# Kernel tuning notes

Hardware: AMD Instinct MI355X
Metric: run time of the kernel (lower is better)

## Reference

```python
import jax, jax.numpy as jnp
import numpy as np

B, C, I, E = 2048, 256, 9, 10


def _contraction(U_list, W_list, x, y):
    """Recursive symmetric contraction for one output irrep.
    U_list/W_list ordered [U1, U2, U3] (correlation 1..3).
    x: [b, c, i], y: [b, e]. Returns flattened [b, c * m].
    """
    U3, W3 = U_list[-1], W_list[-1]
    # main: '...ik,ekc,bci,be->bc...'
    out = jnp.einsum('...ik,ekc,bci,be->bc...', U3, W3, x, y)
    for corr in range(len(U_list) - 2, -1, -1):
        U, W = U_list[corr], W_list[corr]
        # weighting: '...k,ekc,be->bc...'
        c_tensor = jnp.einsum('...k,ekc,be->bc...', U, W, y) + out
        # contract: 'bc...i,bci->bc...'
        out = jnp.einsum('bc...i,bci->bc...', c_tensor, x)
    return out.reshape(out.shape[0], -1)


def setup_inputs() -> dict:
    key = jax.random.key(0)
    ks = jax.random.split(key, 14)
    inp = {
        'x': jax.random.normal(ks[0], (B, C, I), jnp.float32),
        'y': jax.random.uniform(ks[1], (B, E), jnp.float32),
        'U1_s': jax.random.normal(ks[2], (I, 1), jnp.float32),
        'U2_s': jax.random.normal(ks[3], (I, I, 3), jnp.float32),
        'U3_s': jax.random.normal(ks[4], (I, I, I, 23), jnp.float32),
        'U1_v': jax.random.normal(ks[5], (3, I, 1), jnp.float32),
        'U2_v': jax.random.normal(ks[6], (3, I, I, 4), jnp.float32),
        'U3_v': jax.random.normal(ks[7], (3, I, I, I, 30), jnp.float32),
        'W1_s': jax.random.normal(ks[8], (E, 1, C), jnp.float32),
        'W2_s': jax.random.normal(ks[9], (E, 3, C), jnp.float32) / 3.0,
        'W3_s': jax.random.normal(ks[10], (E, 23, C), jnp.float32) / 23.0,
        'W1_v': jax.random.normal(ks[11], (E, 1, C), jnp.float32),
        'W2_v': jax.random.normal(ks[12], (E, 4, C), jnp.float32) / 4.0,
        'W3_v': jax.random.normal(ks[13], (E, 30, C), jnp.float32) / 30.0,
    }
    return inp


def reference(x, y, U1_s, U2_s, U3_s, U1_v, U2_v, U3_v,
              W1_s, W2_s, W3_s, W1_v, W2_v, W3_v):
    out_s = _contraction([U1_s, U2_s, U3_s], [W1_s, W2_s, W3_s], x, y)  # [b, c]
    out_v = _contraction([U1_v, U2_v, U3_v], [W1_v, W2_v, W3_v], x, y)  # [b, c*3]
    return jnp.concatenate([out_s, out_v], axis=-1)  # [b, 4c]
```

## Files before the change

### kernel.cpp

```cpp
#include <hip/hip_runtime.h>
#include <hip/hip_bf16.h>


#define NB 2048
#define NC 256
#define NI 9
#define NE 10

#define N_TRI 165
#define N_PAIR 45
#define BT 8

#define T3N (N_TRI * NE * NC)
#define T2N (N_PAIR * NE * NC)
#define T1N (NI * NE * NC)

__global__ __launch_bounds__(256) void sc_prep(
    const float* __restrict__ U1_s, const float* __restrict__ U2_s,
    const float* __restrict__ U3_s, const float* __restrict__ U1_v,
    const float* __restrict__ U2_v, const float* __restrict__ U3_v,
    const float* __restrict__ W1_s, const float* __restrict__ W2_s,
    const float* __restrict__ W3_s, const float* __restrict__ W1_v,
    const float* __restrict__ W2_v, const float* __restrict__ W3_v,
    float* __restrict__ ws)
{
    const int m = blockIdx.x;
    const int tid = threadIdx.x;
    float4* __restrict__ T3 = (float4*)ws;
    float4* __restrict__ T2 = T3 + T3N;
    float4* __restrict__ T1 = T2 + T2N;

    __shared__ float sym[128];

    if (m < N_TRI) {
        if (tid < 113) {
            int ii = 0, jj = 0, kk = 0, cnt = 0;
            for (int i = 0; i < NI; i++)
                for (int j = i; j < NI; j++)
                    for (int k = j; k < NI; k++) {
                        if (cnt == m) { ii = i; jj = j; kk = k; }
                        cnt++;
                    }
            int P[6][3]; int np;
            if (ii == jj && jj == kk) {
                np = 1;
                P[0][0] = ii; P[0][1] = ii; P[0][2] = ii;
            } else if (ii == jj) {
                np = 3;
                P[0][0] = ii; P[0][1] = ii; P[0][2] = kk;
                P[1][0] = ii; P[1][1] = kk; P[1][2] = ii;
                P[2][0] = kk; P[2][1] = ii; P[2][2] = ii;
            } else if (jj == kk) {
                np = 3;
                P[0][0] = ii; P[0][1] = jj; P[0][2] = jj;
                P[1][0] = jj; P[1][1] = ii; P[1][2] = jj;
                P[2][0] = jj; P[2][1] = jj; P[2][2] = ii;
            } else {
                np = 6;
                P[0][0] = ii; P[0][1] = jj; P[0][2] = kk;
                P[1][0] = ii; P[1][1] = kk; P[1][2] = jj;
                P[2][0] = jj; P[2][1] = ii; P[2][2] = kk;
                P[3][0] = jj; P[3][1] = kk; P[3][2] = ii;
                P[4][0] = kk; P[4][1] = ii; P[4][2] = jj;
                P[5][0] = kk; P[5][1] = jj; P[5][2] = ii;
            }
            float s = 0.f;
            if (tid < 23) {
                for (int p = 0; p < np; p++)
                    s += U3_s[((P[p][0] * NI + P[p][1]) * NI + P[p][2]) * 23 + tid];
            } else {
                int a = (tid - 23) / 30, t = (tid - 23) % 30;
                for (int p = 0; p < np; p++)
                    s += U3_v[(((a * NI + P[p][0]) * NI + P[p][1]) * NI + P[p][2]) * 30 + t];
            }
            sym[tid] = s;
        }
        __syncthreads();
        const int c = tid;
        for (int e = 0; e < NE; e++) {
            float s = 0.f, v0 = 0.f, v1 = 0.f, v2 = 0.f;
            #pragma unroll
            for (int t = 0; t < 23; t++)
                s = fmaf(sym[t], W3_s[(e * 23 + t) * NC + c], s);
            #pragma unroll
            for (int t = 0; t < 30; t++) {
                float wv = W3_v[(e * 30 + t) * NC + c];
                v0 = fmaf(sym[23 + t], wv, v0);
                v1 = fmaf(sym[53 + t], wv, v1);
                v2 = fmaf(sym[83 + t], wv, v2);
            }
            T3[(m * NE + e) * NC + c] = make_float4(s, v0, v1, v2);
        }
    } else if (m < N_TRI + N_PAIR) {
        const int mm = m - N_TRI;
        if (tid < 15) {
            int ii = 0, jj = 0, cnt = 0;
            for (int i = 0; i < NI; i++)
                for (int j = i; j < NI; j++) {
                    if (cnt == mm) { ii = i; jj = j; }
                    cnt++;
                }
            float s;
            if (tid < 3) {
                s = U2_s[(ii * NI + jj) * 3 + tid];
                if (ii != jj) s += U2_s[(jj * NI + ii) * 3 + tid];
            } else {
                int a = (tid - 3) / 4, t = (tid - 3) % 4;
                s = U2_v[((a * NI + ii) * NI + jj) * 4 + t];
                if (ii != jj) s += U2_v[((a * NI + jj) * NI + ii) * 4 + t];
            }
            sym[tid] = s;
        }
        __syncthreads();
        const int c = tid;
        for (int e = 0; e < NE; e++) {
            float s = 0.f, v0 = 0.f, v1 = 0.f, v2 = 0.f;
            #pragma unroll
            for (int t = 0; t < 3; t++)
                s = fmaf(sym[t], W2_s[(e * 3 + t) * NC + c], s);
            #pragma unroll
            for (int t = 0; t < 4; t++) {
                float wv = W2_v[(e * 4 + t) * NC + c];
                v0 = fmaf(sym[3 + t],  wv, v0);
                v1 = fmaf(sym[7 + t],  wv, v1);
                v2 = fmaf(sym[11 + t], wv, v2);
            }
            T2[(mm * NE + e) * NC + c] = make_float4(s, v0, v1, v2);
        }
    } else {
        const int i = m - N_TRI - N_PAIR;
        const int c = tid;
        for (int e = 0; e < NE; e++) {
            float w1s = W1_s[e * NC + c], w1v = W1_v[e * NC + c];
            T1[(i * NE + e) * NC + c] = make_float4(
                U1_s[i] * w1s,
                U1_v[0 * NI + i] * w1v,
                U1_v[1 * NI + i] * w1v,
                U1_v[2 * NI + i] * w1v);
        }
    }
}

__device__ __forceinline__ void tri_advance(int& i, int& j, int& k) {
    k++;
    if (k == NI) { j++; if (j == NI) { i++; j = i; } k = j; }
}

#define ROW_FMA(BUF)                                              \
    {                                                             \
        _Pragma("unroll")                                         \
        for (int e = 0; e < NE; e++) {                            \
            const float4 t = BUF[e];                              \
            _Pragma("unroll")                                     \
            for (int n = 0; n < BT; n++) {                        \
                const float p = w[e][n] * phi[n];                 \
                acc[n][0] = fmaf(p, t.x, acc[n][0]);              \
                acc[n][1] = fmaf(p, t.y, acc[n][1]);              \
                acc[n][2] = fmaf(p, t.z, acc[n][2]);              \
                acc[n][3] = fmaf(p, t.w, acc[n][3]);              \
            }                                                     \
        }                                                         \
    }

template <int M0, int M1, int I0, int J0, int K0>
__device__ __forceinline__ void do_triples(
    const float4* __restrict__ T3, int c, const float* __restrict__ xb,
    const float (&w)[NE][BT], float (&acc)[BT][4])
{
    float4 bufA[NE], bufB[NE];
    #pragma unroll
    for (int e = 0; e < NE; e++) bufA[e] = T3[(M0 * NE + e) * NC + c];
    int i = I0, j = J0, k = K0;
    for (int m = M0; m + 1 < M1; m += 2) {
        #pragma unroll
        for (int e = 0; e < NE; e++) bufB[e] = T3[((m + 1) * NE + e) * NC + c];
        {
            float phi[BT];
            #pragma unroll
            for (int n = 0; n < BT; n++)
                phi[n] = xb[(i * BT + n) * 64] * xb[(j * BT + n) * 64]
                       * xb[(k * BT + n) * 64];
            ROW_FMA(bufA)
        }
        tri_advance(i, j, k);
        const int mp = (m + 2 < M1) ? m + 2 : M1 - 1;
        #pragma unroll
        for (int e = 0; e < NE; e++) bufA[e] = T3[(mp * NE + e) * NC + c];
        {
            float phi[BT];
            #pragma unroll
            for (int n = 0; n < BT; n++)
                phi[n] = xb[(i * BT + n) * 64] * xb[(j * BT + n) * 64]
                       * xb[(k * BT + n) * 64];
            ROW_FMA(bufB)
        }
        tri_advance(i, j, k);
    }
    if ((M1 - M0) & 1) {
        float phi[BT];
        #pragma unroll
        for (int n = 0; n < BT; n++)
            phi[n] = xb[(i * BT + n) * 64] * xb[(j * BT + n) * 64]
                   * xb[(k * BT + n) * 64];
        ROW_FMA(bufA)
    }
}

__global__ __launch_bounds__(256) void sc_main(
    const float* __restrict__ x, const float* __restrict__ y,
    const float* __restrict__ ws, float* __restrict__ out)
{
    const int tid = threadIdx.x;
    const int tx  = tid & 63;
    const int wv  = __builtin_amdgcn_readfirstlane(tid >> 6);
    const int bid = blockIdx.x;
    const int xcd    = bid & 7;
    const int c_tile = xcd >> 1;
    const int b_tile = ((bid >> 3) << 1) | (xcd & 1);
    const int c0 = c_tile << 6;
    const int c  = c0 + tx;
    const int b0 = b_tile << 3;

    __shared__ float xs[NI][BT][64];
    __shared__ float red[BT][4][64];

    #pragma unroll
    for (int p = 0; p < 2; p++) {
        const int pair = tid + p * 256;
        const int n = pair >> 6, cc = pair & 63;
        const float* xp = x + ((size_t)(b0 + n) * NC + c0 + cc) * NI;
        #pragma unroll
        for (int i = 0; i < NI; i++) xs[i][n][cc] = xp[i];
    }
    __syncthreads();
    const float* xb = &xs[0][0][tx];

    float w[NE][BT];
    #pragma unroll
    for (int n = 0; n < BT; n++)
        #pragma unroll
        for (int e = 0; e < NE; e++) w[e][n] = y[(b0 + n) * NE + e];

    float acc[BT][4];
    #pragma unroll
    for (int n = 0; n < BT; n++)
        #pragma unroll
        for (int h = 0; h < 4; h++) acc[n][h] = 0.f;

    const float4* __restrict__ T3 = (const float4*)ws;
    const float4* __restrict__ T2 = T3 + T3N;
    const float4* __restrict__ T1 = T2 + T2N;

    if (wv == 0) {
        do_triples<0, 55, 0, 0, 0>(T3, c, xb, w, acc);
    } else if (wv == 1) {
        do_triples<55, 110, 1, 2, 4>(T3, c, xb, w, acc);
    } else if (wv == 2) {
        do_triples<110, N_TRI, 3, 3, 4>(T3, c, xb, w, acc);
    } else {
        {
            float4 bufA[NE], bufB[NE];
            #pragma unroll
            for (int e = 0; e < NE; e++) bufA[e] = T2[e * NC + c];
            int i = 0, j = 0;
            for (int m = 0; m + 1 < N_PAIR; m += 2) {
                #pragma unroll
                for (int e = 0; e < NE; e++) bufB[e] = T2[((m + 1) * NE + e) * NC + c];
                {
                    float phi[BT];
                    #pragma unroll
                    for (int n = 0; n < BT; n++)
                        phi[n] = xb[(i * BT + n) * 64] * xb[(j * BT + n) * 64];
                    ROW_FMA(bufA)
                }
                j++; if (j == NI) { i++; j = i; }
                const int mp = (m + 2 < N_PAIR) ? m + 2 : N_PAIR - 1;
                #pragma unroll
                for (int e = 0; e < NE; e++) bufA[e] = T2[(mp * NE + e) * NC + c];
                {
                    float phi[BT];
                    #pragma unroll
                    for (int n = 0; n < BT; n++)
                        phi[n] = xb[(i * BT + n) * 64] * xb[(j * BT + n) * 64];
                    ROW_FMA(bufB)
                }
                j++; if (j == NI) { i++; j = i; }
            }
            {
                float phi[BT];
                #pragma unroll
                for (int n = 0; n < BT; n++)
                    phi[n] = xb[(i * BT + n) * 64] * xb[(j * BT + n) * 64];
                ROW_FMA(bufA)
            }
        }
        for (int i = 0; i < NI; i++) {
            float4 tc[NE];
            #pragma unroll
            for (int e = 0; e < NE; e++) tc[e] = T1[(i * NE + e) * NC + c];
            float phi[BT];
            #pragma unroll
            for (int n = 0; n < BT; n++) phi[n] = xb[(i * BT + n) * 64];
            ROW_FMA(tc)
        }
    }

    if (wv == 0) {
        #pragma unroll
        for (int n = 0; n < BT; n++)
            #pragma unroll
            for (int h = 0; h < 4; h++) red[n][h][tx] = acc[n][h];
    }
    __syncthreads();
    if (wv == 1) {
        #pragma unroll
        for (int n = 0; n < BT; n++)
            #pragma unroll
            for (int h = 0; h < 4; h++) acc[n][h] += red[n][h][tx];
    }
    __syncthreads();
    if (wv == 1) {
        #pragma unroll
        for (int n = 0; n < BT; n++)
            #pragma unroll
            for (int h = 0; h < 4; h++) red[n][h][tx] = acc[n][h];
    }
    __syncthreads();
    if (wv == 2) {
        #pragma unroll
        for (int n = 0; n < BT; n++)
            #pragma unroll
            for (int h = 0; h < 4; h++) acc[n][h] += red[n][h][tx];
    }
    __syncthreads();
    if (wv == 2) {
        #pragma unroll
        for (int n = 0; n < BT; n++)
            #pragma unroll
            for (int h = 0; h < 4; h++) red[n][h][tx] = acc[n][h];
    }
    __syncthreads();
    if (wv == 3) {
        #pragma unroll
        for (int n = 0; n < BT; n++) {
            float* ob = out + (size_t)(b0 + n) * (4 * NC);
            ob[c]              = acc[n][0] + red[n][0][tx];
            ob[NC + 3 * c + 0] = acc[n][1] + red[n][1][tx];
            ob[NC + 3 * c + 1] = acc[n][2] + red[n][2][tx];
            ob[NC + 3 * c + 2] = acc[n][3] + red[n][3][tx];
        }
    }
}

extern "C" void kernel_launch(void* const* d_in, const int* in_sizes, int n_in,
                              void* d_out, int out_size, void* d_ws, size_t ws_size,
                              hipStream_t stream) {
    const float* x    = (const float*)d_in[0];
    const float* y    = (const float*)d_in[1];
    const float* U1_s = (const float*)d_in[2];
    const float* U2_s = (const float*)d_in[3];
    const float* U3_s = (const float*)d_in[4];
    const float* U1_v = (const float*)d_in[5];
    const float* U2_v = (const float*)d_in[6];
    const float* U3_v = (const float*)d_in[7];
    const float* W1_s = (const float*)d_in[8];
    const float* W2_s = (const float*)d_in[9];
    const float* W3_s = (const float*)d_in[10];
    const float* W1_v = (const float*)d_in[11];
    const float* W2_v = (const float*)d_in[12];
    const float* W3_v = (const float*)d_in[13];
    float* out = (float*)d_out;
    float* ws  = (float*)d_ws;

    sc_prep<<<N_TRI + N_PAIR + NI, 256, 0, stream>>>(
        U1_s, U2_s, U3_s, U1_v, U2_v, U3_v,
        W1_s, W2_s, W3_s, W1_v, W2_v, W3_v, ws);
    sc_main<<<1024, 256, 0, stream>>>(x, y, ws, out);
}
```

Baseline: 270.9 us.

## Split contraction work across two blocks per tile and parallelize prep over e

The prep kernel gains a second grid dimension over e, so each block computes one e slice instead of looping over all ten. The main kernel becomes a split version that launches twice as many blocks, each handling half of the triple/pair/single rows. One half writes a partial output to workspace and a combine kernel adds it into the final output. This is meant to raise occupancy and balance per-wave work, at the cost of an extra kernel launch, an extra output round trip through memory, and recomputing the x/y staging in both halves. The original single-pass kernel is kept as a fallback when the workspace is too small.

```diff
diff --git a/kernel.cpp b/kernel.cpp
--- a/kernel.cpp
+++ b/kernel.cpp
@@ -14,6 +14,7 @@
 #define T3N (N_TRI * NE * NC)
 #define T2N (N_PAIR * NE * NC)
 #define T1N (NI * NE * NC)
+#define TBYTES ((size_t)(T3N + T2N + T1N) * 16)
 
 __global__ __launch_bounds__(256) void sc_prep(
     const float* __restrict__ U1_s, const float* __restrict__ U2_s,
@@ -25,6 +26,7 @@
     float* __restrict__ ws)
 {
     const int m = blockIdx.x;
+    const int e = blockIdx.y;
     const int tid = threadIdx.x;
     float4* __restrict__ T3 = (float4*)ws;
     float4* __restrict__ T2 = T3 + T3N;
@@ -77,20 +79,18 @@
         }
         __syncthreads();
         const int c = tid;
-        for (int e = 0; e < NE; e++) {
-            float s = 0.f, v0 = 0.f, v1 = 0.f, v2 = 0.f;
-            #pragma unroll
-            for (int t = 0; t < 23; t++)
-                s = fmaf(sym[t], W3_s[(e * 23 + t) * NC + c], s);
-            #pragma unroll
-            for (int t = 0; t < 30; t++) {
-                float wv = W3_v[(e * 30 + t) * NC + c];
-                v0 = fmaf(sym[23 + t], wv, v0);
-                v1 = fmaf(sym[53 + t], wv, v1);
-                v2 = fmaf(sym[83 + t], wv, v2);
-            }
-            T3[(m * NE + e) * NC + c] = make_float4(s, v0, v1, v2);
-        }
+        float s = 0.f, v0 = 0.f, v1 = 0.f, v2 = 0.f;
+        #pragma unroll
+        for (int t = 0; t < 23; t++)
+            s = fmaf(sym[t], W3_s[(e * 23 + t) * NC + c], s);
+        #pragma unroll
+        for (int t = 0; t < 30; t++) {
+            float wv = W3_v[(e * 30 + t) * NC + c];
+            v0 = fmaf(sym[23 + t], wv, v0);
+            v1 = fmaf(sym[53 + t], wv, v1);
+            v2 = fmaf(sym[83 + t], wv, v2);
+        }
+        T3[(m * NE + e) * NC + c] = make_float4(s, v0, v1, v2);
     } else if (m < N_TRI + N_PAIR) {
         const int mm = m - N_TRI;
         if (tid < 15) {
@@ -113,31 +113,27 @@
         }
         __syncthreads();
         const int c = tid;
-        for (int e = 0; e < NE; e++) {
-            float s = 0.f, v0 = 0.f, v1 = 0.f, v2 = 0.f;
-            #pragma unroll
-            for (int t = 0; t < 3; t++)
-                s = fmaf(sym[t], W2_s[(e * 3 + t) * NC + c], s);
-            #pragma unroll
-            for (int t = 0; t < 4; t++) {
-                float wv = W2_v[(e * 4 + t) * NC + c];
-                v0 = fmaf(sym[3 + t],  wv, v0);
-                v1 = fmaf(sym[7 + t],  wv, v1);
-                v2 = fmaf(sym[11 + t], wv, v2);
-            }
-            T2[(mm * NE + e) * NC + c] = make_float4(s, v0, v1, v2);
-        }
+        float s = 0.f, v0 = 0.f, v1 = 0.f, v2 = 0.f;
+        #pragma unroll
+        for (int t = 0; t < 3; t++)
+            s = fmaf(sym[t], W2_s[(e * 3 + t) * NC + c], s);
+        #pragma unroll
+        for (int t = 0; t < 4; t++) {
+            float wv = W2_v[(e * 4 + t) * NC + c];
+            v0 = fmaf(sym[3 + t],  wv, v0);
+            v1 = fmaf(sym[7 + t],  wv, v1);
+            v2 = fmaf(sym[11 + t], wv, v2);
+        }
+        T2[(mm * NE + e) * NC + c] = make_float4(s, v0, v1, v2);
     } else {
         const int i = m - N_TRI - N_PAIR;
         const int c = tid;
-        for (int e = 0; e < NE; e++) {
-            float w1s = W1_s[e * NC + c], w1v = W1_v[e * NC + c];
-            T1[(i * NE + e) * NC + c] = make_float4(
-                U1_s[i] * w1s,
-                U1_v[0 * NI + i] * w1v,
-                U1_v[1 * NI + i] * w1v,
-                U1_v[2 * NI + i] * w1v);
-        }
+        float w1s = W1_s[e * NC + c], w1v = W1_v[e * NC + c];
+        T1[(i * NE + e) * NC + c] = make_float4(
+            U1_s[i] * w1s,
+            U1_v[0 * NI + i] * w1v,
+            U1_v[1 * NI + i] * w1v,
+            U1_v[2 * NI + i] * w1v);
     }
 }
 
@@ -206,7 +202,173 @@
     }
 }
 
-__global__ __launch_bounds__(256) void sc_main(
+template <int M0, int M1, int I0, int J0>
+__device__ __forceinline__ void do_pairs(
+    const float4* __restrict__ T2, int c, const float* __restrict__ xb,
+    const float (&w)[NE][BT], float (&acc)[BT][4])
+{
+    float4 bufA[NE], bufB[NE];
+    #pragma unroll
+    for (int e = 0; e < NE; e++) bufA[e] = T2[(M0 * NE + e) * NC + c];
+    int i = I0, j = J0;
+    for (int m = M0; m + 1 < M1; m += 2) {
+        #pragma unroll
+        for (int e = 0; e < NE; e++) bufB[e] = T2[((m + 1) * NE + e) * NC + c];
+        {
+            float phi[BT];
+            #pragma unroll
+            for (int n = 0; n < BT; n++)
+                phi[n] = xb[(i * BT + n) * 64] * xb[(j * BT + n) * 64];
+            ROW_FMA(bufA)
+        }
+        j++; if (j == NI) { i++; j = i; }
+        const int mp = (m + 2 < M1) ? m + 2 : M1 - 1;
+        #pragma unroll
+        for (int e = 0; e < NE; e++) bufA[e] = T2[(mp * NE + e) * NC + c];
+        {
+            float phi[BT];
+            #pragma unroll
+            for (int n = 0; n < BT; n++)
+                phi[n] = xb[(i * BT + n) * 64] * xb[(j * BT + n) * 64];
+            ROW_FMA(bufB)
+        }
+        j++; if (j == NI) { i++; j = i; }
+    }
+    if ((M1 - M0) & 1) {
+        float phi[BT];
+        #pragma unroll
+        for (int n = 0; n < BT; n++)
+            phi[n] = xb[(i * BT + n) * 64] * xb[(j * BT + n) * 64];
+        ROW_FMA(bufA)
+    }
+}
+
+__device__ __forceinline__ void do_singles(
+    const float4* __restrict__ T1, int c, const float* __restrict__ xb,
+    const float (&w)[NE][BT], float (&acc)[BT][4])
+{
+    for (int i = 0; i < NI; i++) {
+        float4 tc[NE];
+        #pragma unroll
+        for (int e = 0; e < NE; e++) tc[e] = T1[(i * NE + e) * NC + c];
+        float phi[BT];
+        #pragma unroll
+        for (int n = 0; n < BT; n++) phi[n] = xb[(i * BT + n) * 64];
+        ROW_FMA(tc)
+    }
+}
+
+__global__ __launch_bounds__(256) void sc_main_split(
+    const float* __restrict__ x, const float* __restrict__ y,
+    const float* __restrict__ ws, float* __restrict__ out,
+    float* __restrict__ pout)
+{
+    const int tid = threadIdx.x;
+    const int tx  = tid & 63;
+    const int wv  = __builtin_amdgcn_readfirstlane(tid >> 6);
+    const int bx  = blockIdx.x;
+    const int xcd    = bx & 7;
+    const int c_tile = xcd >> 1;
+    const int half   = (bx >> 3) & 1;
+    const int b_tile = ((bx >> 4) << 1) | (xcd & 1);
+    const int c0 = c_tile << 6;
+    const int c  = c0 + tx;
+    const int b0 = b_tile << 3;
+
+    __shared__ float xs[NI][BT][64];
+    __shared__ float red[BT][4][64];
+
+    #pragma unroll
+    for (int p = 0; p < 2; p++) {
+        const int pair = tid + p * 256;
+        const int n = pair >> 6, cc = pair & 63;
+        const float* xp = x + ((size_t)(b0 + n) * NC + c0 + cc) * NI;
+        #pragma unroll
+        for (int i = 0; i < NI; i++) xs[i][n][cc] = xp[i];
+    }
+    __syncthreads();
+    const float* xb = &xs[0][0][tx];
+
+    float w[NE][BT];
+    #pragma unroll
+    for (int n = 0; n < BT; n++)
+        #pragma unroll
+        for (int e = 0; e < NE; e++) w[e][n] = y[(b0 + n) * NE + e];
+
+    float acc[BT][4];
+    #pragma unroll
+    for (int n = 0; n < BT; n++)
+        #pragma unroll
+        for (int h = 0; h < 4; h++) acc[n][h] = 0.f;
+
+    const float4* __restrict__ T3 = (const float4*)ws;
+    const float4* __restrict__ T2 = T3 + T3N;
+    const float4* __restrict__ T1 = T2 + T2N;
+
+    if (half == 0) {
+        if      (wv == 0) do_triples<0,   27, 0, 0, 0>(T3, c, xb, w, acc);
+        else if (wv == 1) do_triples<27,  55, 0, 3, 6>(T3, c, xb, w, acc);
+        else if (wv == 2) do_triples<55,  83, 1, 2, 4>(T3, c, xb, w, acc);
+        else              do_triples<83, 110, 2, 2, 4>(T3, c, xb, w, acc);
+    } else {
+        if      (wv == 0) do_triples<110, 138, 3, 3, 4>(T3, c, xb, w, acc);
+        else if (wv == 1) do_triples<138, 165, 4, 5, 8>(T3, c, xb, w, acc);
+        else if (wv == 2) do_pairs<0, 27, 0, 0>(T2, c, xb, w, acc);
+        else {
+            do_pairs<27, 45, 3, 6>(T2, c, xb, w, acc);
+            do_singles(T1, c, xb, w, acc);
+        }
+    }
+
+    if (wv == 0) {
+        #pragma unroll
+        for (int n = 0; n < BT; n++)
+            #pragma unroll
+            for (int h = 0; h < 4; h++) red[n][h][tx] = acc[n][h];
+    }
+    __syncthreads();
+    if (wv == 1) {
+        #pragma unroll
+        for (int n = 0; n < BT; n++)
+            #pragma unroll
+            for (int h = 0; h < 4; h++) acc[n][h] += red[n][h][tx];
+    }
+    __syncthreads();
+    if (wv == 1) {
+        #pragma unroll
+        for (int n = 0; n < BT; n++)
+            #pragma unroll
+            for (int h = 0; h < 4; h++) red[n][h][tx] = acc[n][h];
+    }
+    __syncthreads();
+    if (wv == 2) {
+        #pragma unroll
+        for (int n = 0; n < BT; n++)
+            #pragma unroll
+            for (int h = 0; h < 4; h++) acc[n][h] += red[n][h][tx];
+    }
+    __syncthreads();
+    if (wv == 2) {
+        #pragma unroll
+        for (int n = 0; n < BT; n++)
+            #pragma unroll
+            for (int h = 0; h < 4; h++) red[n][h][tx] = acc[n][h];
+    }
+    __syncthreads();
+    if (wv == 3) {
+        float* __restrict__ dst = half ? out : pout;
+        #pragma unroll
+        for (int n = 0; n < BT; n++) {
+            float* ob = dst + (size_t)(b0 + n) * (4 * NC);
+            ob[c]              = acc[n][0] + red[n][0][tx];
+            ob[NC + 3 * c + 0] = acc[n][1] + red[n][1][tx];
+            ob[NC + 3 * c + 1] = acc[n][2] + red[n][2][tx];
+            ob[NC + 3 * c + 2] = acc[n][3] + red[n][3][tx];
+        }
+    }
+}
+
+__global__ __launch_bounds__(256) void sc_main_full(
     const float* __restrict__ x, const float* __restrict__ y,
     const float* __restrict__ ws, float* __restrict__ out)
 {
@@ -251,58 +413,12 @@
     const float4* __restrict__ T2 = T3 + T3N;
     const float4* __restrict__ T1 = T2 + T2N;
 
-    if (wv == 0) {
-        do_triples<0, 55, 0, 0, 0>(T3, c, xb, w, acc);
-    } else if (wv == 1) {
-        do_triples<55, 110, 1, 2, 4>(T3, c, xb, w, acc);
-    } else if (wv == 2) {
-        do_triples<110, N_TRI, 3, 3, 4>(T3, c, xb, w, acc);
-    } else {
-        {
-            float4 bufA[NE], bufB[NE];
-            #pragma unroll
-            for (int e = 0; e < NE; e++) bufA[e] = T2[e * NC + c];
-            int i = 0, j = 0;
-            for (int m = 0; m + 1 < N_PAIR; m += 2) {
-                #pragma unroll
-                for (int e = 0; e < NE; e++) bufB[e] = T2[((m + 1) * NE + e) * NC + c];
-                {
-                    float phi[BT];
-                    #pragma unroll
-                    for (int n = 0; n < BT; n++)
-                        phi[n] = xb[(i * BT + n) * 64] * xb[(j * BT + n) * 64];
-                    ROW_FMA(bufA)
-                }
-                j++; if (j == NI) { i++; j = i; }
-                const int mp = (m + 2 < N_PAIR) ? m + 2 : N_PAIR - 1;
-                #pragma unroll
-                for (int e = 0; e < NE; e++) bufA[e] = T2[(mp * NE + e) * NC + c];
-                {
-                    float phi[BT];
-                    #pragma unroll
-                    for (int n = 0; n < BT; n++)
-                        phi[n] = xb[(i * BT + n) * 64] * xb[(j * BT + n) * 64];
-                    ROW_FMA(bufB)
-                }
-                j++; if (j == NI) { i++; j = i; }
-            }
-            {
-                float phi[BT];
-                #pragma unroll
-                for (int n = 0; n < BT; n++)
-                    phi[n] = xb[(i * BT + n) * 64] * xb[(j * BT + n) * 64];
-                ROW_FMA(bufA)
-            }
-        }
-        for (int i = 0; i < NI; i++) {
-            float4 tc[NE];
-            #pragma unroll
-            for (int e = 0; e < NE; e++) tc[e] = T1[(i * NE + e) * NC + c];
-            float phi[BT];
-            #pragma unroll
-            for (int n = 0; n < BT; n++) phi[n] = xb[(i * BT + n) * 64];
-            ROW_FMA(tc)
-        }
+    if      (wv == 0) do_triples<0,   55, 0, 0, 0>(T3, c, xb, w, acc);
+    else if (wv == 1) do_triples<55, 110, 1, 2, 4>(T3, c, xb, w, acc);
+    else if (wv == 2) do_triples<110, N_TRI, 3, 3, 4>(T3, c, xb, w, acc);
+    else {
+        do_pairs<0, N_PAIR, 0, 0>(T2, c, xb, w, acc);
+        do_singles(T1, c, xb, w, acc);
     }
 
     if (wv == 0) {
@@ -349,6 +465,16 @@
             ob[NC + 3 * c + 1] = acc[n][2] + red[n][2][tx];
             ob[NC + 3 * c + 2] = acc[n][3] + red[n][3][tx];
         }
+    }
+}
+
+__global__ __launch_bounds__(256) void sc_combine(
+    float4* __restrict__ out, const float4* __restrict__ p, int n4)
+{
+    int i = blockIdx.x * 256 + threadIdx.x;
+    if (i < n4) {
+        float4 a = out[i], b = p[i];
+        out[i] = make_float4(a.x + b.x, a.y + b.y, a.z + b.z, a.w + b.w);
     }
 }
 
@@ -372,8 +498,18 @@
     float* out = (float*)d_out;
     float* ws  = (float*)d_ws;
 
-    sc_prep<<<N_TRI + N_PAIR + NI, 256, 0, stream>>>(
+    sc_prep<<<dim3(N_TRI + N_PAIR + NI, NE), 256, 0, stream>>>(
         U1_s, U2_s, U3_s, U1_v, U2_v, U3_v,
         W1_s, W2_s, W3_s, W1_v, W2_v, W3_v, ws);
-    sc_main<<<1024, 256, 0, stream>>>(x, y, ws, out);
-}
+
+    const size_t out_bytes = (size_t)out_size * sizeof(float);
+    if (ws_size >= TBYTES + out_bytes) {
+        float* pout = (float*)((char*)d_ws + TBYTES);
+        sc_main_split<<<2048, 256, 0, stream>>>(x, y, ws, out, pout);
+        const int n4 = out_size / 4;
+        sc_combine<<<(n4 + 255) / 256, 256, 0, stream>>>(
+            (float4*)out, (const float4*)pout, n4);
+    } else {
+        sc_main_full<<<1024, 256, 0, stream>>>(x, y, ws, out);
+    }
+}
```

Measured after the change: 386.4 us. 42.6% more time.
